# Optimization experiments

Measured on AMD Instinct MI355X. Metric: run time of the kernel, lower is better.

Reference implementation:

```python
import jax, jax.numpy as jnp
import numpy as np
from itertools import combinations

A = 4          # anchor_points
K = 16         # neighbor_num
INTRA = A * (A - 1) // 2   # 6
CH = INTRA * 2 + A * A     # 28 = generator channels
B, N, S = 1, 8192, 4096
CIN, COUT = 64, 128


def cdist(x):
    # pairwise euclidean distances [B,N,N], zero-safe sqrt (zero grad at d=0)
    sq = jnp.sum(x * x, -1)
    d2 = sq[:, :, None] + sq[:, None, :] - 2.0 * jnp.einsum('bnc,bmc->bnm', x, x)
    d2 = jnp.maximum(d2, 0.0)
    m = d2 > 0
    return jnp.where(m, jnp.sqrt(jnp.where(m, d2, 1.0)), 0.0)


def index_points(points, idx):
    # points [B,N,...], idx [B,*] -> [B,*,...]
    return jax.vmap(lambda p, i: p[i])(points, idx)


def index_points_dists(dists, i1, i2):
    # dists [B,N,N]; result[b,...] = dists[b, i1[b,...], i2[b,...]]
    i1, i2 = jnp.broadcast_arrays(i1, i2)
    return jax.vmap(lambda d, a, b: d[a, b])(dists, i1, i2)


def generator(xyz):
    # RotationInvariantDistFea.forward(xyz, concat_raw_relative_fea=True)
    D = cdist(xyz)
    neg_nd, ni = jax.lax.top_k(-D, K)   # K >= A; smallest-K, sorted ascending
    nd = -neg_nd
    ai = ni[:, :, :A]
    # intra-anchor dists: dists to anchors 1..A-1 plus pairwise dists among them
    subs = [index_points_dists(D, ai[:, :, pi], ai[:, :, pj])[:, :, None]
            for pi, pj in combinations(range(1, A), 2)]
    intra = jnp.concatenate([nd[:, :, 1:A]] + subs, axis=2)  # [B,P,6]
    # inter-anchor dists: center anchors x neighbor anchors -> [B,P,K,A*A]
    nai = index_points(ai, ni)                                # [B,P,K,A]
    inter = index_points_dists(D, ai[:, :, None, :, None],
                               nai[:, :, :, None, :]).reshape(D.shape[0], D.shape[1], K, A * A)
    center = jnp.broadcast_to(intra[:, :, None, :], (intra.shape[0], intra.shape[1], K, INTRA))
    rf = jnp.concatenate([center, index_points(intra, ni), inter], axis=3)  # [B,P,K,28]
    return rf, ni, D


def mlp(x, W, b, g, be, act):
    # Linear + BatchNorm1d (training mode: stats over batch*points) + optional leaky_relu(0.2)
    y = x @ W + b
    mu = jnp.mean(y, (0, 1))
    var = jnp.var(y, (0, 1))
    y = (y - mu) * jax.lax.rsqrt(var + 1e-5) * g + be
    return jax.nn.leaky_relu(y, 0.2) if act else y


def forward(xyz, feature, sample_indexes, Ww, bw, gw, betaw, Wb, bb, gb, betab, Wo, bo, go, betao):
    rf_before, ni_before, D_before = generator(xyz)
    intra_before = rf_before[:, :, 0, :INTRA]
    xyz_s = index_points(xyz, sample_indexes)
    feat = index_points(feature, sample_indexes)
    intra_before = index_points(intra_before, sample_indexes)
    rf_after, ni_after, _ = generator(xyz_s)
    intra_after = rf_after[:, :, 0, :INTRA]
    a_before = index_points(ni_before[:, :, :A], sample_indexes)                  # [B,S,A]
    a_after = jax.vmap(lambda s, a: s[a])(sample_indexes, ni_after[:, :, :A])     # map to global idx
    inter = index_points_dists(D_before, a_before[:, :, :, None],
                               a_after[:, :, None, :]).reshape(B, S, A * A)
    adf = jnp.concatenate([intra_before, intra_after, inter], axis=2)             # [B,S,28]
    w = mlp(adf, Ww, bw, gw, betaw, False)
    bia = mlp(adf, Wb, bb, gb, betab, False)
    feat = jax.nn.leaky_relu(feat * w + bia, 0.2)
    feat = jnp.concatenate([feat, adf], axis=2)                                   # [B,S,92]
    feat = mlp(feat, Wo, bo, go, betao, True)                                     # [B,S,128]
    return xyz_s, feat, rf_after, ni_after


def setup_inputs():
    key = jax.random.key(0)
    ks = jax.random.split(key, 8)
    xyz = jax.random.normal(ks[0], (B, N, 3), jnp.float32)
    feature = jax.random.normal(ks[1], (B, N, CIN), jnp.float32)
    sample_indexes = jnp.stack([jax.random.permutation(jax.random.fold_in(ks[2], i), N)[:S]
                                for i in range(B)]).astype(jnp.int32)

    def lin(k, cin, cout):
        k1, k2 = jax.random.split(k)
        W = jax.random.normal(k1, (cin, cout), jnp.float32) / np.float32(np.sqrt(cin))
        b = jax.random.normal(k2, (cout,), jnp.float32) * 0.01
        return W, b, jnp.ones((cout,), jnp.float32), jnp.zeros((cout,), jnp.float32)

    Ww, bw, gw, betaw = lin(ks[5], CH, CIN)
    Wb, bb, gb, betab = lin(ks[6], CH, CIN)
    Wo, bo, go, betao = lin(ks[7], CH + CIN, COUT)
    return dict(xyz=xyz, feature=feature, sample_indexes=sample_indexes,
                Ww=Ww, bw=bw, gw=gw, betaw=betaw,
                Wb=Wb, bb=bb, gb=gb, betab=betab,
                Wo=Wo, bo=bo, go=go, betao=betao)


def reference(xyz, feature, sample_indexes, Ww, bw, gw, betaw, Wb, bb, gb, betab, Wo, bo, go, betao):
    return forward(xyz, feature, sample_indexes, Ww, bw, gw, betaw, Wb, bb, gb, betab, Wo, bo, go, betao)
```

## Files before the change

### kernel.cpp

```cpp
#include <hip/hip_runtime.h>
#include <hip/hip_bf16.h>
#include <math.h>

#define N_PTS 8192
#define S_PTS 4096
#define CAP 256
typedef unsigned long long u64;
typedef unsigned u32;

__device__ __forceinline__ float pair_dist_d(const float4 a, const float4 b) {
    double ax = a.x, ay = a.y, az = a.z;
    double bx = b.x, by = b.y, bz = b.z;
    double dx = ax - bx, dy = ay - by, dz = az - bz;
    double d2 = dx * dx + dy * dy + dz * dz;
    return d2 > 0.0 ? (float)sqrt(d2) : 0.0f;
}

__device__ __forceinline__ float d2_f32_gram(const float4 a, const float4 b) {
    float dot = __fadd_rn(__fadd_rn(__fmul_rn(a.x, b.x), __fmul_rn(a.y, b.y)),
                          __fmul_rn(a.z, b.z));
    float d2 = __fsub_rn(__fadd_rn(a.w, b.w), __fmul_rn(2.0f, dot));
    return fmaxf(d2, 0.0f);
}

__device__ __forceinline__ u32 bitonic64_u32(u32 v, int lane) {
#pragma unroll
    for (int k = 2; k <= 64; k <<= 1) {
#pragma unroll
        for (int j2 = k >> 1; j2 >= 1; j2 >>= 1) {
            u32 o = __shfl_xor(v, j2, 64);
            bool keepMin = (((lane & j2) == 0) == ((lane & k) == 0));
            bool less = o < v;
            v = keepMin ? (less ? o : v) : (less ? v : o);
        }
    }
    return v;
}

__device__ __forceinline__ u64 bitonic64_u64(u64 v, int lane) {
#pragma unroll
    for (int k = 2; k <= 64; k <<= 1) {
#pragma unroll
        for (int j2 = k >> 1; j2 >= 1; j2 >>= 1) {
            u64 o = __shfl_xor(v, j2, 64);
            bool keepMin = (((lane & j2) == 0) == ((lane & k) == 0));
            bool less = o < v;
            v = keepMin ? (less ? o : v) : (less ? v : o);
        }
    }
    return v;
}

__global__ __launch_bounds__(256) void stage_kernel(
        const float* __restrict__ xyz, const int* __restrict__ sidx,
        float4* __restrict__ cb, float4* __restrict__ ca,
        float* __restrict__ out_xyz_s) {
    int i = blockIdx.x * blockDim.x + threadIdx.x;
    if (i < N_PTS) {
        float x = xyz[i * 3 + 0], y = xyz[i * 3 + 1], z = xyz[i * 3 + 2];
        float sq = __fadd_rn(__fadd_rn(__fmul_rn(x, x), __fmul_rn(y, y)),
                             __fmul_rn(z, z));
        cb[i] = make_float4(x, y, z, sq);
    }
    if (i < S_PTS) {
        int si = sidx[i];
        float x = xyz[si * 3 + 0], y = xyz[si * 3 + 1], z = xyz[si * 3 + 2];
        float sq = __fadd_rn(__fadd_rn(__fmul_rn(x, x), __fmul_rn(y, y)),
                             __fmul_rn(z, z));
        ca[i] = make_float4(x, y, z, sq);
        out_xyz_s[i * 3 + 0] = x;
        out_xyz_s[i * 3 + 1] = y;
        out_xyz_s[i * 3 + 2] = z;
    }
}

template <int K>
__device__ u64 rescan_topk(const float4 q, const float4* __restrict__ pts,
                           int n, int lane) {
    u64 res = ~0ull;
    u64 prev = 0;
    for (int r = 0; r < K; ++r) {
        u64 best = ~0ull;
        for (int c = lane; c < n; c += 64) {
            float d2 = d2_f32_gram(q, pts[c]);
            float D = d2 > 0.0f ? __fsqrt_rn(d2) : 0.0f;
            u64 key = ((u64)__float_as_uint(D) << 32) | (u64)(u32)c;
            bool ok = (r == 0) || (key > prev);
            if (ok && key < best) best = key;
        }
#pragma unroll
        for (int off = 32; off >= 1; off >>= 1) {
            u64 o = __shfl_xor(best, off, 64);
            best = (o < best) ? o : best;
        }
        if (lane == r) res = best;
        prev = best;
    }
    return res;
}

template <int K>
__device__ u64 finalize_sort(const u64* buf, u32 cnt, int lane) {
    if (cnt <= 64u) {
        u64 v = (lane < (int)cnt) ? buf[lane] : ~0ull;
        return bitonic64_u64(v, lane);
    }
    u64 L0 = ~0ull, L1 = ~0ull, L2 = ~0ull, L3 = ~0ull;
    for (u32 mm = lane; mm < cnt; mm += 64) {
        u64 kk = buf[mm];
        if (kk < L3) {
            if (kk < L1) {
                L3 = L2; L2 = L1;
                if (kk < L0) { L1 = L0; L0 = kk; } else L1 = kk;
            } else {
                if (kk < L2) { L3 = L2; L2 = kk; } else L3 = kk;
            }
        }
    }
    u64 res = ~0ull;
#pragma unroll
    for (int r = 0; r < K; ++r) {
        u64 mr = L0;
#pragma unroll
        for (int off = 32; off >= 1; off >>= 1) {
            u64 o = __shfl_xor(mr, off, 64);
            mr = (o < mr) ? o : mr;
        }
        if (lane == r) res = mr;
        if (L0 == mr) { L0 = L1; L1 = L2; L2 = L3; L3 = ~0ull; }
    }
    return res;
}

__global__ __launch_bounds__(256) void knn_kernel(
        const float4* __restrict__ cb, const float4* __restrict__ ca,
        const int* __restrict__ sidx,
        int* __restrict__ a_before, float* __restrict__ intra_before,
        int* __restrict__ ni_i, float* __restrict__ intra_after,
        float* __restrict__ out_ni) {
    __shared__ u32 smin[8][256];
    __shared__ u64 sbuf[8][CAP];
    __shared__ u32 staus[8];
    __shared__ u32 scnt[8];
    __shared__ float4 sq[4];
    int t = threadIdx.x, lane = t & 63, wid = t >> 6;
    int s0 = blockIdx.x * 4;
    if (t < 4) sq[t] = cb[sidx[s0 + t]];
    if (t < 8) scnt[t] = 0;
    __syncthreads();
    float4 q[4];
#pragma unroll
    for (int i = 0; i < 4; ++i) q[i] = sq[i];

    u32 mB[4], mA[4];
#pragma unroll
    for (int i = 0; i < 4; ++i) { mB[i] = ~0u; mA[i] = ~0u; }
    for (int c = t; c < N_PTS; c += 256) {
        float4 p = cb[c];
#pragma unroll
        for (int i = 0; i < 4; ++i) {
            u32 b = __float_as_uint(d2_f32_gram(q[i], p));
            mB[i] = b < mB[i] ? b : mB[i];
        }
    }
    for (int c = t; c < S_PTS; c += 256) {
        float4 p = ca[c];
#pragma unroll
        for (int i = 0; i < 4; ++i) {
            u32 b = __float_as_uint(d2_f32_gram(q[i], p));
            mA[i] = b < mA[i] ? b : mA[i];
        }
    }
#pragma unroll
    for (int i = 0; i < 4; ++i) { smin[i][t] = mB[i]; smin[4 + i][t] = mA[i]; }
    __syncthreads();
#pragma unroll
    for (int m = 0; m < 2; ++m) {
        int st = (m == 0) ? wid : wid + 4;
        u32 v = smin[st][lane];
        u32 v2 = smin[st][lane + 64];  v = v2 < v ? v2 : v;
        v2 = smin[st][lane + 128];     v = v2 < v ? v2 : v;
        v2 = smin[st][lane + 192];     v = v2 < v ? v2 : v;
        v = bitonic64_u32(v, lane);
        int kk = (st < 4) ? 3 : 15;
        if (lane == kk) staus[st] = v;
    }
    __syncthreads();
    u32 tB[4], tA[4];
#pragma unroll
    for (int i = 0; i < 4; ++i) { tB[i] = staus[i]; tA[i] = staus[4 + i]; }

    for (int c = t; c < N_PTS; c += 256) {
        float4 p = cb[c];
#pragma unroll
        for (int i = 0; i < 4; ++i) {
            u32 b = __float_as_uint(d2_f32_gram(q[i], p));
            if (b <= tB[i]) {
                float d2v = __uint_as_float(b);
                float D = d2v > 0.0f ? __fsqrt_rn(d2v) : 0.0f;
                u32 pos = atomicAdd(&scnt[i], 1u);
                if (pos < CAP)
                    sbuf[i][pos] = ((u64)__float_as_uint(D) << 32) | (u64)(u32)c;
            }
        }
    }
    for (int c = t; c < S_PTS; c += 256) {
        float4 p = ca[c];
#pragma unroll
        for (int i = 0; i < 4; ++i) {
            u32 b = __float_as_uint(d2_f32_gram(q[i], p));
            if (b <= tA[i]) {
                float d2v = __uint_as_float(b);
                float D = d2v > 0.0f ? __fsqrt_rn(d2v) : 0.0f;
                u32 pos = atomicAdd(&scnt[4 + i], 1u);
                if (pos < CAP)
                    sbuf[4 + i][pos] = ((u64)__float_as_uint(D) << 32) | (u64)(u32)c;
            }
        }
    }
    __syncthreads();
    {
        int s = s0 + wid;
        float4 qq = q[wid];
        u32 cnt = scnt[wid];
        u64 res = (cnt <= CAP) ? finalize_sort<4>(sbuf[wid], cnt, lane)
                               : rescan_topk<4>(qq, cb, N_PTS, lane);
        int idx = (int)(res & 0xffffffffull);
        if (lane < 4) a_before[s * 4 + lane] = idx;
        if (lane >= 1 && lane < 4)
            intra_before[s * 6 + (lane - 1)] = pair_dist_d(qq, cb[idx]);
        int i1 = __shfl(idx, 1, 64);
        int i2 = __shfl(idx, 2, 64);
        int i3 = __shfl(idx, 3, 64);
        if (lane < 3) {
            int pa = (lane == 2) ? i2 : i1;
            int pb = (lane == 0) ? i2 : i3;
            intra_before[s * 6 + 3 + lane] = pair_dist_d(cb[pa], cb[pb]);
        }
        cnt = scnt[4 + wid];
        res = (cnt <= CAP) ? finalize_sort<16>(sbuf[4 + wid], cnt, lane)
                           : rescan_topk<16>(qq, ca, S_PTS, lane);
        idx = (int)(res & 0xffffffffull);
        if (lane < 16) {
            ni_i[s * 16 + lane] = idx;
            out_ni[s * 16 + lane] = (float)idx;
        }
        if (lane >= 1 && lane < 4)
            intra_after[s * 6 + (lane - 1)] = pair_dist_d(qq, ca[idx]);
        i1 = __shfl(idx, 1, 64);
        i2 = __shfl(idx, 2, 64);
        i3 = __shfl(idx, 3, 64);
        if (lane < 3) {
            int pa = (lane == 2) ? i2 : i1;
            int pb = (lane == 0) ? i2 : i3;
            intra_after[s * 6 + 3 + lane] = pair_dist_d(ca[pa], ca[pb]);
        }
    }
}

__global__ __launch_bounds__(256) void assemble_kernel(
        const float4* __restrict__ ca, const float4* __restrict__ cb,
        const int* __restrict__ ni_i, const float* __restrict__ intra_after,
        const int* __restrict__ a_before, const float* __restrict__ intra_before,
        const int* __restrict__ sidx,
        float* __restrict__ out_rf, float* __restrict__ adf) {
    __shared__ int s_ni[4][16];
    __shared__ float s_rf[4][16 * 28];
    __shared__ float s_ia[4][8];
    int t = threadIdx.x, wid = t >> 6, lane = t & 63;
    int s = blockIdx.x * 4 + wid;
    if (lane < 16) s_ni[wid][lane] = ni_i[s * 16 + lane];
    if (lane < 6) s_ia[wid][lane] = intra_after[s * 6 + lane];
    __syncthreads();

    int k = lane >> 2, qq = lane & 3;
    int nai_q = ni_i[s_ni[wid][k] * 16 + qq];
    float4 pq = ca[nai_q];
#pragma unroll
    for (int p = 0; p < 4; ++p) {
        float4 pp = ca[s_ni[wid][p]];
        s_rf[wid][k * 28 + 12 + p * 4 + qq] = pair_dist_d(pp, pq);
    }
    for (int idx = lane; idx < 16 * 12; idx += 64) {
        int kk = idx / 12, c = idx % 12;
        float v = (c < 6) ? s_ia[wid][c] : intra_after[s_ni[wid][kk] * 6 + (c - 6)];
        s_rf[wid][kk * 28 + c] = v;
    }
    if (lane < 16) {
        int p = lane >> 2, q2 = lane & 3;
        int ib = a_before[s * 4 + p];
        int ia = sidx[s_ni[wid][q2]];
        adf[s * 28 + 12 + lane] = pair_dist_d(cb[ib], cb[ia]);
    } else if (lane >= 32 && lane < 38) {
        adf[s * 28 + (lane - 32)] = intra_before[s * 6 + (lane - 32)];
    } else if (lane >= 40 && lane < 46) {
        adf[s * 28 + 6 + (lane - 40)] = s_ia[wid][lane - 40];
    }
    __syncthreads();
    const int base = s * 16 * 28;
    for (int idx = lane; idx < 16 * 28; idx += 64) out_rf[base + idx] = s_rf[wid][idx];
}

__global__ __launch_bounds__(256) void mlp1_kernel(
        const float* __restrict__ adf,
        const float* __restrict__ Ww, const float* __restrict__ bw,
        const float* __restrict__ Wb, const float* __restrict__ bb,
        float* __restrict__ y_wb) {
    __shared__ float sW[28 * 128];
    __shared__ float sb[128];
    __shared__ float sA[16 * 28];
    int t = threadIdx.x;
    for (int i = t; i < 28 * 128; i += 256) {
        int k = i >> 7, c = i & 127;
        sW[i] = (c < 64) ? Ww[k * 64 + c] : Wb[k * 64 + (c - 64)];
    }
    if (t < 128) sb[t] = (t < 64) ? bw[t] : bb[t - 64];
    int s0 = blockIdx.x * 16;
    for (int i = t; i < 16 * 28; i += 256) sA[i] = adf[s0 * 28 + i];
    __syncthreads();
    int sl = t >> 4, grp = t & 15;
    int s = s0 + sl;
    float acc[8];
#pragma unroll
    for (int k = 0; k < 8; ++k) acc[k] = sb[grp * 8 + k];
    for (int k2 = 0; k2 < 28; ++k2) {
        float a = sA[sl * 28 + k2];
        float4 w0 = *(const float4*)&sW[k2 * 128 + grp * 8];
        float4 w1 = *(const float4*)&sW[k2 * 128 + grp * 8 + 4];
        acc[0] = fmaf(a, w0.x, acc[0]);
        acc[1] = fmaf(a, w0.y, acc[1]);
        acc[2] = fmaf(a, w0.z, acc[2]);
        acc[3] = fmaf(a, w0.w, acc[3]);
        acc[4] = fmaf(a, w1.x, acc[4]);
        acc[5] = fmaf(a, w1.y, acc[5]);
        acc[6] = fmaf(a, w1.z, acc[6]);
        acc[7] = fmaf(a, w1.w, acc[7]);
    }
#pragma unroll
    for (int k = 0; k < 8; ++k) y_wb[(grp * 8 + k) * 4096 + s] = acc[k];
}

__global__ __launch_bounds__(256) void stats_kernel(
        const float* __restrict__ y,
        const float* __restrict__ g0, const float* __restrict__ be0,
        const float* __restrict__ g1, const float* __restrict__ be1, int csplit,
        float* __restrict__ scale, float* __restrict__ shift) {
    int c = blockIdx.x;
    const float* p = y + c * 4096;
    float s1 = 0.0f, s2 = 0.0f;
    for (int i = threadIdx.x; i < 4096; i += 256) {
        float v = p[i];
        s1 += v;
        s2 = fmaf(v, v, s2);
    }
    __shared__ float l1[256], l2[256];
    l1[threadIdx.x] = s1;
    l2[threadIdx.x] = s2;
    __syncthreads();
    for (int off = 128; off; off >>= 1) {
        if (threadIdx.x < off) {
            l1[threadIdx.x] += l1[threadIdx.x + off];
            l2[threadIdx.x] += l2[threadIdx.x + off];
        }
        __syncthreads();
    }
    if (threadIdx.x == 0) {
        float mean = l1[0] * (1.0f / 4096.0f);
        float var = l2[0] * (1.0f / 4096.0f) - mean * mean;
        float g = (c < csplit) ? g0[c] : g1[c - csplit];
        float be = (c < csplit) ? be0[c] : be1[c - csplit];
        float sc = g / sqrtf(var + 1e-5f);
        scale[c] = sc;
        shift[c] = be - mean * sc;
    }
}

__global__ __launch_bounds__(256) void mlp2_kernel(
        const float* __restrict__ y_wb,
        const float* __restrict__ scale1, const float* __restrict__ shift1,
        const float* __restrict__ feature, const int* __restrict__ sidx,
        const float* __restrict__ adf,
        const float* __restrict__ Wo, const float* __restrict__ bo,
        float* __restrict__ y_o) {
    __shared__ float sW[92 * 128];
    __shared__ float t2[16 * 129];
    __shared__ float scat[16 * 92];
    int t = threadIdx.x;
    int s0 = blockIdx.x * 16;
    for (int i = t; i < 92 * 128; i += 256) sW[i] = Wo[i];
    for (int i = t; i < 16 * 128; i += 256) {
        int row = i & 15, c = i >> 4;
        t2[row * 129 + c] = fmaf(y_wb[c * 4096 + s0 + row], scale1[c], shift1[c]);
    }
    __syncthreads();
    for (int rr = 0; rr < 16; rr += 4) {
        int r = rr + (t >> 6);
        int c = t & 63;
        int si = sidx[s0 + r];
        float f = feature[si * 64 + c];
        float v = fmaf(f, t2[r * 129 + c], t2[r * 129 + 64 + c]);
        scat[r * 92 + c] = v >= 0.0f ? v : 0.2f * v;
    }
    for (int i = t; i < 16 * 28; i += 256) {
        int row = i / 28, k = i % 28;
        scat[row * 92 + 64 + k] = adf[(s0 + row) * 28 + k];
    }
    __syncthreads();
    int r = t >> 4, cg = t & 15;
    float acc[8];
#pragma unroll
    for (int j = 0; j < 8; ++j) acc[j] = bo[cg * 8 + j];
    for (int c = 0; c < 92; ++c) {
        float a = scat[r * 92 + c];
        float4 w0 = *(const float4*)&sW[c * 128 + cg * 8];
        float4 w1 = *(const float4*)&sW[c * 128 + cg * 8 + 4];
        acc[0] = fmaf(a, w0.x, acc[0]);
        acc[1] = fmaf(a, w0.y, acc[1]);
        acc[2] = fmaf(a, w0.z, acc[2]);
        acc[3] = fmaf(a, w0.w, acc[3]);
        acc[4] = fmaf(a, w1.x, acc[4]);
        acc[5] = fmaf(a, w1.y, acc[5]);
        acc[6] = fmaf(a, w1.z, acc[6]);
        acc[7] = fmaf(a, w1.w, acc[7]);
    }
    int s = s0 + r;
#pragma unroll
    for (int j = 0; j < 8; ++j) y_o[(cg * 8 + j) * 4096 + s] = acc[j];
}

__global__ __launch_bounds__(256) void final_kernel(
        const float* __restrict__ y_o,
        const float* __restrict__ scale, const float* __restrict__ shift,
        float* __restrict__ out_feat) {
    int tid = blockIdx.x * 256 + threadIdx.x;
    int j = tid >> 12;
    int s = tid & 4095;
    float v = fmaf(y_o[tid], scale[j], shift[j]);
    v = v >= 0.0f ? v : 0.2f * v;
    out_feat[s * 128 + j] = v;
}

extern "C" void kernel_launch(void* const* d_in, const int* in_sizes, int n_in,
                              void* d_out, int out_size, void* d_ws, size_t ws_size,
                              hipStream_t stream) {
    const float* xyz = (const float*)d_in[0];
    const float* feature = (const float*)d_in[1];
    const int* sidx = (const int*)d_in[2];
    const float* Ww = (const float*)d_in[3];
    const float* bw = (const float*)d_in[4];
    const float* gw = (const float*)d_in[5];
    const float* betaw = (const float*)d_in[6];
    const float* Wb = (const float*)d_in[7];
    const float* bb = (const float*)d_in[8];
    const float* gb = (const float*)d_in[9];
    const float* betab = (const float*)d_in[10];
    const float* Wo = (const float*)d_in[11];
    const float* bo = (const float*)d_in[12];
    const float* go = (const float*)d_in[13];
    const float* betao = (const float*)d_in[14];

    float* out = (float*)d_out;
    float* out_xyz = out;
    float* out_feat = out + 12288;
    float* out_rf = out + 12288 + 524288;
    float* out_ni = out + 12288 + 524288 + 1835008;

    float* ws = (float*)d_ws;
    float4* cb = (float4*)ws;
    float4* ca = (float4*)(ws + 32768);
    int* a_before = (int*)(ws + 49152);
    float* intra_before = ws + 65536;
    int* ni_i = (int*)(ws + 90112);
    float* intra_after = ws + 155648;
    float* adf = ws + 180224;
    float* y_wb = ws + 294912;
    float* y_o = ws + 819200;
    float* scale1 = ws + 1343488;
    float* shift1 = ws + 1343616;
    float* scale_o = ws + 1343744;
    float* shift_o = ws + 1343872;

    stage_kernel<<<32, 256, 0, stream>>>(xyz, sidx, cb, ca, out_xyz);
    knn_kernel<<<1024, 256, 0, stream>>>(cb, ca, sidx, a_before, intra_before,
                                         ni_i, intra_after, out_ni);
    assemble_kernel<<<1024, 256, 0, stream>>>(ca, cb, ni_i, intra_after, a_before,
                                              intra_before, sidx, out_rf, adf);
    mlp1_kernel<<<256, 256, 0, stream>>>(adf, Ww, bw, Wb, bb, y_wb);
    stats_kernel<<<128, 256, 0, stream>>>(y_wb, gw, betaw, gb, betab, 64, scale1, shift1);
    mlp2_kernel<<<256, 256, 0, stream>>>(y_wb, scale1, shift1, feature, sidx, adf, Wo, bo, y_o);
    stats_kernel<<<128, 256, 0, stream>>>(y_o, go, betao, go, betao, 128, scale_o, shift_o);
    final_kernel<<<2048, 256, 0, stream>>>(y_o, scale_o, shift_o, out_feat);
}
```

Measured before the change: 182.8 us.

## Unroll kNN scans by four, fuse assemble with mlp1, fuse stats into final

The kNN distance scans now load four points per iteration, combine mins in a tree, and skip the candidate-append branch when none of the four pass the threshold. The assemble kernel now also computes the first linear layer from shared memory, which removes the separate mlp1 launch. The second BN stats kernel is merged into the final kernel, one block per channel, removing another launch. In exchange, every assemble block reloads the 28x128 weights, and the final kernel's transposed stores with a stride of 128 floats are poorly coalesced and run on only 128 blocks.

Measured after the change: 181.9 us. About the same (-0.5%).

```diff
diff --git a/kernel.cpp b/kernel.cpp
--- a/kernel.cpp
+++ b/kernel.cpp
@@ -155,20 +155,38 @@
     u32 mB[4], mA[4];
 #pragma unroll
     for (int i = 0; i < 4; ++i) { mB[i] = ~0u; mA[i] = ~0u; }
-    for (int c = t; c < N_PTS; c += 256) {
-        float4 p = cb[c];
+    for (int c = t; c < N_PTS; c += 1024) {
+        float4 p0 = cb[c];
+        float4 p1 = cb[c + 256];
+        float4 p2 = cb[c + 512];
+        float4 p3 = cb[c + 768];
 #pragma unroll
         for (int i = 0; i < 4; ++i) {
-            u32 b = __float_as_uint(d2_f32_gram(q[i], p));
-            mB[i] = b < mB[i] ? b : mB[i];
-        }
-    }
-    for (int c = t; c < S_PTS; c += 256) {
-        float4 p = ca[c];
+            u32 b0 = __float_as_uint(d2_f32_gram(q[i], p0));
+            u32 b1 = __float_as_uint(d2_f32_gram(q[i], p1));
+            u32 b2 = __float_as_uint(d2_f32_gram(q[i], p2));
+            u32 b3 = __float_as_uint(d2_f32_gram(q[i], p3));
+            u32 m01 = b0 < b1 ? b0 : b1;
+            u32 m23 = b2 < b3 ? b2 : b3;
+            u32 m = m01 < m23 ? m01 : m23;
+            mB[i] = m < mB[i] ? m : mB[i];
+        }
+    }
+    for (int c = t; c < S_PTS; c += 1024) {
+        float4 p0 = ca[c];
+        float4 p1 = ca[c + 256];
+        float4 p2 = ca[c + 512];
+        float4 p3 = ca[c + 768];
 #pragma unroll
         for (int i = 0; i < 4; ++i) {
-            u32 b = __float_as_uint(d2_f32_gram(q[i], p));
-            mA[i] = b < mA[i] ? b : mA[i];
+            u32 b0 = __float_as_uint(d2_f32_gram(q[i], p0));
+            u32 b1 = __float_as_uint(d2_f32_gram(q[i], p1));
+            u32 b2 = __float_as_uint(d2_f32_gram(q[i], p2));
+            u32 b3 = __float_as_uint(d2_f32_gram(q[i], p3));
+            u32 m01 = b0 < b1 ? b0 : b1;
+            u32 m23 = b2 < b3 ? b2 : b3;
+            u32 m = m01 < m23 ? m01 : m23;
+            mA[i] = m < mA[i] ? m : mA[i];
         }
     }
 #pragma unroll
@@ -190,31 +208,57 @@
 #pragma unroll
     for (int i = 0; i < 4; ++i) { tB[i] = staus[i]; tA[i] = staus[4 + i]; }
 
-    for (int c = t; c < N_PTS; c += 256) {
-        float4 p = cb[c];
+    for (int c = t; c < N_PTS; c += 1024) {
+        float4 p0 = cb[c];
+        float4 p1 = cb[c + 256];
+        float4 p2 = cb[c + 512];
+        float4 p3 = cb[c + 768];
 #pragma unroll
         for (int i = 0; i < 4; ++i) {
-            u32 b = __float_as_uint(d2_f32_gram(q[i], p));
-            if (b <= tB[i]) {
-                float d2v = __uint_as_float(b);
-                float D = d2v > 0.0f ? __fsqrt_rn(d2v) : 0.0f;
-                u32 pos = atomicAdd(&scnt[i], 1u);
-                if (pos < CAP)
-                    sbuf[i][pos] = ((u64)__float_as_uint(D) << 32) | (u64)(u32)c;
+            u32 b0 = __float_as_uint(d2_f32_gram(q[i], p0));
+            u32 b1 = __float_as_uint(d2_f32_gram(q[i], p1));
+            u32 b2 = __float_as_uint(d2_f32_gram(q[i], p2));
+            u32 b3 = __float_as_uint(d2_f32_gram(q[i], p3));
+            if (b0 <= tB[i] || b1 <= tB[i] || b2 <= tB[i] || b3 <= tB[i]) {
+#pragma unroll
+                for (int u = 0; u < 4; ++u) {
+                    u32 b = (u == 0) ? b0 : (u == 1) ? b1 : (u == 2) ? b2 : b3;
+                    if (b <= tB[i]) {
+                        float d2v = __uint_as_float(b);
+                        float D = d2v > 0.0f ? __fsqrt_rn(d2v) : 0.0f;
+                        u32 pos = atomicAdd(&scnt[i], 1u);
+                        if (pos < CAP)
+                            sbuf[i][pos] = ((u64)__float_as_uint(D) << 32) |
+                                           (u64)(u32)(c + 256 * u);
+                    }
+                }
             }
         }
     }
-    for (int c = t; c < S_PTS; c += 256) {
-        float4 p = ca[c];
+    for (int c = t; c < S_PTS; c += 1024) {
+        float4 p0 = ca[c];
+        float4 p1 = ca[c + 256];
+        float4 p2 = ca[c + 512];
+        float4 p3 = ca[c + 768];
 #pragma unroll
         for (int i = 0; i < 4; ++i) {
-            u32 b = __float_as_uint(d2_f32_gram(q[i], p));
-            if (b <= tA[i]) {
-                float d2v = __uint_as_float(b);
-                float D = d2v > 0.0f ? __fsqrt_rn(d2v) : 0.0f;
-                u32 pos = atomicAdd(&scnt[4 + i], 1u);
-                if (pos < CAP)
-                    sbuf[4 + i][pos] = ((u64)__float_as_uint(D) << 32) | (u64)(u32)c;
+            u32 b0 = __float_as_uint(d2_f32_gram(q[i], p0));
+            u32 b1 = __float_as_uint(d2_f32_gram(q[i], p1));
+            u32 b2 = __float_as_uint(d2_f32_gram(q[i], p2));
+            u32 b3 = __float_as_uint(d2_f32_gram(q[i], p3));
+            if (b0 <= tA[i] || b1 <= tA[i] || b2 <= tA[i] || b3 <= tA[i]) {
+#pragma unroll
+                for (int u = 0; u < 4; ++u) {
+                    u32 b = (u == 0) ? b0 : (u == 1) ? b1 : (u == 2) ? b2 : b3;
+                    if (b <= tA[i]) {
+                        float d2v = __uint_as_float(b);
+                        float D = d2v > 0.0f ? __fsqrt_rn(d2v) : 0.0f;
+                        u32 pos = atomicAdd(&scnt[4 + i], 1u);
+                        if (pos < CAP)
+                            sbuf[4 + i][pos] = ((u64)__float_as_uint(D) << 32) |
+                                               (u64)(u32)(c + 256 * u);
+                    }
+                }
             }
         }
     }
@@ -258,17 +302,28 @@
     }
 }
 
-__global__ __launch_bounds__(256) void assemble_kernel(
+__global__ __launch_bounds__(256) void asm_mlp1_kernel(
         const float4* __restrict__ ca, const float4* __restrict__ cb,
         const int* __restrict__ ni_i, const float* __restrict__ intra_after,
         const int* __restrict__ a_before, const float* __restrict__ intra_before,
         const int* __restrict__ sidx,
-        float* __restrict__ out_rf, float* __restrict__ adf) {
+        const float* __restrict__ Ww, const float* __restrict__ bw,
+        const float* __restrict__ Wb, const float* __restrict__ bb,
+        float* __restrict__ out_rf, float* __restrict__ adf,
+        float* __restrict__ y_wb) {
     __shared__ int s_ni[4][16];
-    __shared__ float s_rf[4][16 * 28];
+    __shared__ float s_rf[4][448];
     __shared__ float s_ia[4][8];
+    __shared__ float s_adf[4][28];
+    __shared__ float sW[28 * 128];
+    __shared__ float sb[128];
     int t = threadIdx.x, wid = t >> 6, lane = t & 63;
     int s = blockIdx.x * 4 + wid;
+    for (int i = t; i < 28 * 128; i += 256) {
+        int k = i >> 7, c = i & 127;
+        sW[i] = (c < 64) ? Ww[k * 64 + c] : Wb[k * 64 + (c - 64)];
+    }
+    if (t < 128) sb[t] = (t < 64) ? bw[t] : bb[t - 64];
     if (lane < 16) s_ni[wid][lane] = ni_i[s * 16 + lane];
     if (lane < 6) s_ia[wid][lane] = intra_after[s * 6 + lane];
     __syncthreads();
@@ -290,54 +345,31 @@
         int p = lane >> 2, q2 = lane & 3;
         int ib = a_before[s * 4 + p];
         int ia = sidx[s_ni[wid][q2]];
-        adf[s * 28 + 12 + lane] = pair_dist_d(cb[ib], cb[ia]);
+        float v = pair_dist_d(cb[ib], cb[ia]);
+        adf[s * 28 + 12 + lane] = v;
+        s_adf[wid][12 + lane] = v;
     } else if (lane >= 32 && lane < 38) {
-        adf[s * 28 + (lane - 32)] = intra_before[s * 6 + (lane - 32)];
+        float v = intra_before[s * 6 + (lane - 32)];
+        adf[s * 28 + (lane - 32)] = v;
+        s_adf[wid][lane - 32] = v;
     } else if (lane >= 40 && lane < 46) {
-        adf[s * 28 + 6 + (lane - 40)] = s_ia[wid][lane - 40];
-    }
-    __syncthreads();
+        float v = s_ia[wid][lane - 40];
+        adf[s * 28 + 6 + (lane - 40)] = v;
+        s_adf[wid][6 + (lane - 40)] = v;
+    }
     const int base = s * 16 * 28;
     for (int idx = lane; idx < 16 * 28; idx += 64) out_rf[base + idx] = s_rf[wid][idx];
-}
-
-__global__ __launch_bounds__(256) void mlp1_kernel(
-        const float* __restrict__ adf,
-        const float* __restrict__ Ww, const float* __restrict__ bw,
-        const float* __restrict__ Wb, const float* __restrict__ bb,
-        float* __restrict__ y_wb) {
-    __shared__ float sW[28 * 128];
-    __shared__ float sb[128];
-    __shared__ float sA[16 * 28];
-    int t = threadIdx.x;
-    for (int i = t; i < 28 * 128; i += 256) {
-        int k = i >> 7, c = i & 127;
-        sW[i] = (c < 64) ? Ww[k * 64 + c] : Wb[k * 64 + (c - 64)];
-    }
-    if (t < 128) sb[t] = (t < 64) ? bw[t] : bb[t - 64];
-    int s0 = blockIdx.x * 16;
-    for (int i = t; i < 16 * 28; i += 256) sA[i] = adf[s0 * 28 + i];
-    __syncthreads();
-    int sl = t >> 4, grp = t & 15;
-    int s = s0 + sl;
-    float acc[8];
-#pragma unroll
-    for (int k = 0; k < 8; ++k) acc[k] = sb[grp * 8 + k];
-    for (int k2 = 0; k2 < 28; ++k2) {
-        float a = sA[sl * 28 + k2];
-        float4 w0 = *(const float4*)&sW[k2 * 128 + grp * 8];
-        float4 w1 = *(const float4*)&sW[k2 * 128 + grp * 8 + 4];
-        acc[0] = fmaf(a, w0.x, acc[0]);
-        acc[1] = fmaf(a, w0.y, acc[1]);
-        acc[2] = fmaf(a, w0.z, acc[2]);
-        acc[3] = fmaf(a, w0.w, acc[3]);
-        acc[4] = fmaf(a, w1.x, acc[4]);
-        acc[5] = fmaf(a, w1.y, acc[5]);
-        acc[6] = fmaf(a, w1.z, acc[6]);
-        acc[7] = fmaf(a, w1.w, acc[7]);
-    }
-#pragma unroll
-    for (int k = 0; k < 8; ++k) y_wb[(grp * 8 + k) * 4096 + s] = acc[k];
+    __syncthreads();
+    int sb0 = blockIdx.x * 4;
+#pragma unroll
+    for (int o = t; o < 512; o += 256) {
+        int r = o >> 7, c = o & 127;
+        float acc = sb[c];
+#pragma unroll
+        for (int k2 = 0; k2 < 28; ++k2)
+            acc = fmaf(s_adf[r][k2], sW[k2 * 128 + c], acc);
+        y_wb[c * 4096 + sb0 + r] = acc;
+    }
 }
 
 __global__ __launch_bounds__(256) void stats_kernel(
@@ -430,14 +462,42 @@
 
 __global__ __launch_bounds__(256) void final_kernel(
         const float* __restrict__ y_o,
-        const float* __restrict__ scale, const float* __restrict__ shift,
+        const float* __restrict__ go, const float* __restrict__ betao,
         float* __restrict__ out_feat) {
-    int tid = blockIdx.x * 256 + threadIdx.x;
-    int j = tid >> 12;
-    int s = tid & 4095;
-    float v = fmaf(y_o[tid], scale[j], shift[j]);
-    v = v >= 0.0f ? v : 0.2f * v;
-    out_feat[s * 128 + j] = v;
+    int j = blockIdx.x;
+    const float* p = y_o + j * 4096;
+    float s1 = 0.0f, s2 = 0.0f;
+    for (int i = threadIdx.x; i < 4096; i += 256) {
+        float v = p[i];
+        s1 += v;
+        s2 = fmaf(v, v, s2);
+    }
+    __shared__ float l1[256], l2[256];
+    __shared__ float ssc, ssh;
+    l1[threadIdx.x] = s1;
+    l2[threadIdx.x] = s2;
+    __syncthreads();
+    for (int off = 128; off; off >>= 1) {
+        if (threadIdx.x < off) {
+            l1[threadIdx.x] += l1[threadIdx.x + off];
+            l2[threadIdx.x] += l2[threadIdx.x + off];
+        }
+        __syncthreads();
+    }
+    if (threadIdx.x == 0) {
+        float mean = l1[0] * (1.0f / 4096.0f);
+        float var = l2[0] * (1.0f / 4096.0f) - mean * mean;
+        float sc = go[j] / sqrtf(var + 1e-5f);
+        ssc = sc;
+        ssh = betao[j] - mean * sc;
+    }
+    __syncthreads();
+    float sc = ssc, sh = ssh;
+    for (int i = threadIdx.x; i < 4096; i += 256) {
+        float v = fmaf(p[i], sc, sh);
+        v = v >= 0.0f ? v : 0.2f * v;
+        out_feat[i * 128 + j] = v;
+    }
 }
 
 extern "C" void kernel_launch(void* const* d_in, const int* in_sizes, int n_in,
@@ -477,17 +537,14 @@
     float* y_o = ws + 819200;
     float* scale1 = ws + 1343488;
     float* shift1 = ws + 1343616;
-    float* scale_o = ws + 1343744;
-    float* shift_o = ws + 1343872;
 
     stage_kernel<<<32, 256, 0, stream>>>(xyz, sidx, cb, ca, out_xyz);
     knn_kernel<<<1024, 256, 0, stream>>>(cb, ca, sidx, a_before, intra_before,
                                          ni_i, intra_after, out_ni);
-    assemble_kernel<<<1024, 256, 0, stream>>>(ca, cb, ni_i, intra_after, a_before,
-                                              intra_before, sidx, out_rf, adf);
-    mlp1_kernel<<<256, 256, 0, stream>>>(adf, Ww, bw, Wb, bb, y_wb);
+    asm_mlp1_kernel<<<1024, 256, 0, stream>>>(ca, cb, ni_i, intra_after, a_before,
+                                              intra_before, sidx, Ww, bw, Wb, bb,
+                                              out_rf, adf, y_wb);
     stats_kernel<<<128, 256, 0, stream>>>(y_wb, gw, betaw, gb, betab, 64, scale1, shift1);
     mlp2_kernel<<<256, 256, 0, stream>>>(y_wb, scale1, shift1, feature, sidx, adf, Wo, bo, y_o);
-    stats_kernel<<<128, 256, 0, stream>>>(y_o, go, betao, go, betao, 128, scale_o, shift_o);
-    final_kernel<<<2048, 256, 0, stream>>>(y_o, scale_o, shift_o, out_feat);
-}
+    final_kernel<<<128, 256, 0, stream>>>(y_o, go, betao, out_feat);
+}
```
